# Performance work log

Hardware: AMD Instinct MI355X
Metric: run time of the kernel (lower is better)

Reference implementation:

```python
import jax, jax.numpy as jnp
import numpy as np

TAU = 10.0 / 7.0
V_TH = 1.0
ALPHA = 10.0  # sigmoid surrogate slope

@jax.custom_vjp
def spike_fn(v):
    # Heaviside(v - v_th) forward, sigmoid surrogate backward
    return (v >= V_TH).astype(v.dtype)

def _spike_fwd(v):
    return spike_fn(v), v

def _spike_bwd(v, g):
    s = jax.nn.sigmoid(ALPHA * (v - V_TH))
    return (g * ALPHA * s * (1.0 - s),)

spike_fn.defvjp(_spike_fwd, _spike_bwd)

def lif_multistep(x_bctm):
    # x: [B, C, T, M]; LIF recurrence over T axis, v_reset=0 hard reset,
    # decay_input=True: v = v + (x - v)/tau
    x_t = jnp.moveaxis(x_bctm, 2, 0)  # [T, B, C, M]
    def step(v, x):
        v = v + (x - v) / TAU
        s = spike_fn(v)
        v = v * (1.0 - s)  # hard reset to 0 (not detached)
        return v, s
    v0 = jnp.zeros_like(x_t[0])
    _, s_t = jax.lax.scan(step, v0, x_t)
    return jnp.moveaxis(s_t, 0, 2)  # [B, C, T, M]

def conv2d(x, w, pad, dil):
    return jax.lax.conv_general_dilated(
        x, w, window_strides=(1, 1),
        padding=[(pad[0], pad[0]), (pad[1], pad[1])],
        rhs_dilation=dil,
        dimension_numbers=('NCHW', 'OIHW', 'NCHW'))

def setup_inputs() -> dict:
    key = jax.random.key(0)
    k0, k1, k2, k3, k4 = jax.random.split(key, 5)
    B, T, M = 32, 128, 40
    x = jax.random.normal(k0, (B, 1, T, M), dtype=jnp.float32)
    # kaiming-ish init: std = 1/sqrt(fan_in)
    w1 = jax.random.normal(k1, (64, 1, 4, 3), dtype=jnp.float32) / np.sqrt(1 * 4 * 3)
    w2 = jax.random.normal(k2, (64, 64, 4, 3), dtype=jnp.float32) / np.sqrt(64 * 4 * 3)
    w3 = jax.random.normal(k3, (64, 64, 4, 3), dtype=jnp.float32) / np.sqrt(64 * 4 * 3)
    kw, kb = jax.random.split(k4)
    wf = jax.random.normal(kw, (12, 64 * 40), dtype=jnp.float32) / np.sqrt(64 * 40)
    bf = jnp.zeros((12,), dtype=jnp.float32)
    return {"x": x, "w1": w1, "w2": w2, "w3": w3, "wf": wf, "bf": bf}

def reference(x, w1, w2, w3, wf, bf):
    h = conv2d(x, w1, (2, 1), (1, 1))     # [B,64,T+1,40]
    h = lif_multistep(h)
    h = conv2d(h, w2, (6, 3), (4, 3))     # shape preserved
    h = lif_multistep(h)
    h = conv2d(h, w3, (24, 9), (16, 9))   # shape preserved
    h = lif_multistep(h)
    B, C, T, M = h.shape
    h = jnp.transpose(h, (0, 2, 1, 3)).reshape(B, T, C * M)  # flatten=True path
    y = h @ wf.T + bf                     # [B, T, 12]
    return y.mean(axis=1)                 # [B, 12]
```

## Files before the change

kernel.cpp:

```cpp
#include <hip/hip_runtime.h>


typedef __attribute__((ext_vector_type(8))) _Float16 v8h;
typedef __attribute__((ext_vector_type(16))) float v16f;
typedef _Float16 half_t;

#define NB 32
#define NC 64
#define NT 129
#define TIN 128
#define NM 40
#define MS8 72
#define ROWB8 2952
#define SROWB8 2560

__global__ void prep_wfrag(const float* __restrict__ w, uint4* __restrict__ wf) {
    int tid = blockIdx.x * 256 + threadIdx.x;
    if (tid >= 12288) return;
    int lane = tid & 63;
    int rest = tid >> 6;
    int hl = rest & 1;
    int ct = (rest >> 1) & 1;
    int cq = (rest >> 2) & 3;
    int tap = rest >> 4;
    int kh = tap / 3, kw = tap % 3;
    int co = ct * 32 + (lane & 31);
    unsigned short o[8];
#pragma unroll
    for (int jj = 0; jj < 8; jj++) {
        int ci = cq * 16 + (lane >> 5) * 8 + jj;
        float wv = w[((co * 64 + ci) * 4 + kh) * 3 + kw];
        _Float16 hi = (_Float16)wv;
        _Float16 val = hl ? (_Float16)((wv - (float)hi) * 2048.0f) : hi;
        unsigned short us;
        __builtin_memcpy(&us, &val, 2);
        o[jj] = us;
    }
    uint4 r;
    __builtin_memcpy(&r, o, 16);
    wf[tid] = r;
}

__global__ void conv1_lif1(const float* __restrict__ x, const float* __restrict__ w1,
                           unsigned char* __restrict__ s1) {
    const int mg = blockIdx.x;
    const int b = blockIdx.y;
    const int c = threadIdx.x & 63;
    const int ml = threadIdx.x >> 6;
    const int m = mg * 4 + ml;
    float w[4][3];
#pragma unroll
    for (int kh = 0; kh < 4; kh++)
#pragma unroll
        for (int kw = 0; kw < 3; kw++) w[kh][kw] = w1[(c * 4 + kh) * 3 + kw];
    const float* xb = x + (size_t)b * TIN * NM;

    float xw[12][3];
#pragma unroll
    for (int rr = 0; rr < 12; rr++)
#pragma unroll
        for (int kw = 0; kw < 3; kw++) xw[rr][kw] = 0.f;
#pragma unroll
    for (int rr = 2; rr < 4; rr++)
#pragma unroll
        for (int kw = 0; kw < 3; kw++) {
            int mc = m - 1 + kw;
            xw[rr][kw] = ((unsigned)mc < (unsigned)NM) ? xb[(rr - 2) * NM + mc] : 0.f;
        }

    unsigned char* orow = s1 + ((size_t)b * NT * NM + m) * 64 + c;
    float v = 0.f;
    const float TAUc = 10.0f / 7.0f;

    for (int tb = 0; tb < NT; tb += 8) {
#pragma unroll
        for (int q = 0; q < 8; q++) {
            int row = tb + 2 + q;
#pragma unroll
            for (int kw = 0; kw < 3; kw++) {
                int mc = m - 1 + kw;
                xw[4 + q][kw] = (row < TIN && (unsigned)mc < (unsigned)NM)
                                    ? xb[row * NM + mc] : 0.f;
            }
        }
        int kmax = (NT - tb) < 8 ? (NT - tb) : 8;
#pragma unroll
        for (int k = 0; k < 8; k++) {
            if (k < kmax) {
                float uacc = 0.f;
#pragma unroll
                for (int kh = 0; kh < 4; kh++)
#pragma unroll
                    for (int kw = 0; kw < 3; kw++) uacc += xw[k + kh][kw] * w[kh][kw];
                v = v + (uacc - v) / TAUc;
                orow[(size_t)(tb + k) * NM * 64] = (v >= 1.0f) ? 1 : 0;
                if (v >= 1.0f) v = 0.0f;
            }
        }
#pragma unroll
        for (int rr = 0; rr < 4; rr++)
#pragma unroll
            for (int kw = 0; kw < 3; kw++) xw[rr][kw] = xw[8 + rr][kw];
    }
}

__device__ inline v8h expand01(uint2 raw) {
    unsigned o0 = __builtin_amdgcn_perm(0u, raw.x, 0x04010400u) * 0x3C00u;
    unsigned o1 = __builtin_amdgcn_perm(0u, raw.x, 0x04030402u) * 0x3C00u;
    unsigned o2 = __builtin_amdgcn_perm(0u, raw.y, 0x04010400u) * 0x3C00u;
    unsigned o3 = __builtin_amdgcn_perm(0u, raw.y, 0x04030402u) * 0x3C00u;
    uint4 o = make_uint4(o0, o1, o2, o3);
    return __builtin_bit_cast(v8h, o);
}

template <int DH, int PH, int DW, int PW, int RMOD>
__global__ __launch_bounds__(256, 2) void convW(const unsigned char* __restrict__ spk,
                                                const uint4* __restrict__ wfrag,
                                                float* __restrict__ u) {
    __shared__ uint2 ldsq[7 * ROWB8 / 8];
    char* lds = (char*)ldsq;
    const int tid = threadIdx.x;
    const int lane = tid & 63;
    const int wv = tid >> 6;
    const int wp = wv >> 1;
    const int hl = wv & 1;
    const int bx = blockIdx.x;
    const int b = blockIdx.y;
    int r, jj0;
    if (bx < 32) { r = bx % RMOD; jj0 = (bx / RMOD) * 4; }
    else         { r = 0;         jj0 = (32 / RMOD) * 4; }

    const char* spb = (const char*)spk + (size_t)b * NT * SROWB8;
#pragma unroll
    for (int k = 0; k < 9; k++) {
        int c = tid + k * 256;
        if (c < 2296) {
            int i = c / 328;
            int rem = c - i * 328;
            int s = rem >> 3;
            int q = rem & 7;
            int tg = r - PH + DH * (jj0 + i);
            uint2 val = make_uint2(0u, 0u);
            if ((unsigned)tg < (unsigned)NT && s < 40)
                val = *(const uint2*)(spb + ((size_t)tg * NM + s) * 64 + q * 8);
            *(uint2*)(lds + i * ROWB8 + s * MS8 + q * 8) = val;
        }
    }
    __syncthreads();

    const int pos = lane & 31;
    const int jl = pos >> 4;
    const int ml = pos & 15;
    const int hseg = lane >> 5;
    const int jj = jj0 + 2 * wp + jl;
    const int ldsrow = 2 * wp + jl;
    const int t = r + DH * jj;
    const int mtb[3] = {0, 16, 24};

    int P[3][3];
#pragma unroll
    for (int mt = 0; mt < 3; mt++)
#pragma unroll
        for (int kw = 0; kw < 3; kw++) {
            int md = mtb[mt] + ml + kw * DW - PW;
            int sel = ((unsigned)md < 40u) ? md : 40;
            P[mt][kw] = ldsrow * ROWB8 + sel * MS8 + hseg * 8;
        }

    v16f acc[3][2];
#pragma unroll
    for (int a = 0; a < 3; a++)
#pragma unroll
        for (int c2 = 0; c2 < 2; c2++) acc[a][c2] = (v16f)(0.0f);

    const int hl64 = hl * 64;
    uint4 cA0[4], cA1[4], nA0[4], nA1[4];
#pragma unroll
    for (int cq = 0; cq < 4; cq++) {
        const uint4* wq = wfrag + cq * 256 + hl64 + lane;
        cA0[cq] = wq[0];
        cA1[cq] = wq[128];
    }

#pragma unroll
    for (int tap = 0; tap < 12; tap++) {
        if (tap < 11) {
#pragma unroll
            for (int cq = 0; cq < 4; cq++) {
                const uint4* wq = wfrag + ((tap + 1) * 4 + cq) * 256 + hl64 + lane;
                nA0[cq] = wq[0];
                nA1[cq] = wq[128];
            }
        }
        const int kh = tap / 3, kw = tap % 3;
#pragma unroll
        for (int cq = 0; cq < 4; cq++) {
            uint2 r0 = *(const uint2*)(lds + P[0][kw] + kh * ROWB8 + cq * 16);
            uint2 r1 = *(const uint2*)(lds + P[1][kw] + kh * ROWB8 + cq * 16);
            uint2 r2 = *(const uint2*)(lds + P[2][kw] + kh * ROWB8 + cq * 16);
            v8h B0 = expand01(r0);
            v8h B1 = expand01(r1);
            v8h B2 = expand01(r2);
            v8h A0 = __builtin_bit_cast(v8h, cA0[cq]);
            v8h A1 = __builtin_bit_cast(v8h, cA1[cq]);
            acc[0][0] = __builtin_amdgcn_mfma_f32_32x32x16_f16(A0, B0, acc[0][0], 0, 0, 0);
            acc[0][1] = __builtin_amdgcn_mfma_f32_32x32x16_f16(A1, B0, acc[0][1], 0, 0, 0);
            acc[1][0] = __builtin_amdgcn_mfma_f32_32x32x16_f16(A0, B1, acc[1][0], 0, 0, 0);
            acc[1][1] = __builtin_amdgcn_mfma_f32_32x32x16_f16(A1, B1, acc[1][1], 0, 0, 0);
            acc[2][0] = __builtin_amdgcn_mfma_f32_32x32x16_f16(A0, B2, acc[2][0], 0, 0, 0);
            acc[2][1] = __builtin_amdgcn_mfma_f32_32x32x16_f16(A1, B2, acc[2][1], 0, 0, 0);
        }
        if (tap < 11) {
#pragma unroll
            for (int cq = 0; cq < 4; cq++) {
                cA0[cq] = nA0[cq];
                cA1[cq] = nA1[cq];
            }
        }
    }

    const float invs = 1.0f / 2048.0f;
    float4* lred = (float4*)lds;
    __syncthreads();
#pragma unroll
    for (int mt = 0; mt < 3; mt++) {
        if (hl) {
#pragma unroll
            for (int ct = 0; ct < 2; ct++)
#pragma unroll
                for (int g = 0; g < 4; g++) {
                    float4 vv;
                    vv.x = acc[mt][ct][4 * g + 0];
                    vv.y = acc[mt][ct][4 * g + 1];
                    vv.z = acc[mt][ct][4 * g + 2];
                    vv.w = acc[mt][ct][4 * g + 3];
                    lred[(wp * 8 + ct * 4 + g) * 64 + lane] = vv;
                }
        }
        __syncthreads();
        if (!hl && t < NT) {
            int m = mtb[mt] + ml;
            float* base = u + ((size_t)(b * NT + t) * NM + m) * 64;
#pragma unroll
            for (int ct = 0; ct < 2; ct++)
#pragma unroll
                for (int g = 0; g < 4; g++) {
                    float4 lo = lred[(wp * 8 + ct * 4 + g) * 64 + lane];
                    int co = ct * 32 + 8 * g + 4 * hseg;
                    float4 val;
                    val.x = acc[mt][ct][4 * g + 0] + lo.x * invs;
                    val.y = acc[mt][ct][4 * g + 1] + lo.y * invs;
                    val.z = acc[mt][ct][4 * g + 2] + lo.z * invs;
                    val.w = acc[mt][ct][4 * g + 3] + lo.w * invs;
                    *(float4*)(base + co) = val;
                }
        }
        __syncthreads();
    }
}

__global__ void lif_spikes(const float* __restrict__ u, unsigned char* __restrict__ s2) {
    int tid = blockIdx.x * 256 + threadIdx.x;
    int b = tid / 2560;
    int cm = tid % 2560;
    const float* up = u + (size_t)b * NT * 2560 + cm;
    unsigned char* sp = s2 + (size_t)b * NT * 2560 + cm;
    float v = 0.f;
    const float TAUc = 10.0f / 7.0f;
    for (int tb = 0; tb < 128; tb += 16) {
        float uu[16];
#pragma unroll
        for (int k = 0; k < 16; k++) uu[k] = up[(size_t)(tb + k) * 2560];
#pragma unroll
        for (int k = 0; k < 16; k++) {
            v = v + (uu[k] - v) / TAUc;
            sp[(size_t)(tb + k) * 2560] = (v >= 1.0f) ? 1 : 0;
            if (v >= 1.0f) v = 0.f;
        }
    }
    float uu = up[(size_t)128 * 2560];
    v = v + (uu - v) / TAUc;
    sp[(size_t)128 * 2560] = (v >= 1.0f) ? 1 : 0;
}

__global__ void lif_sum(const float* __restrict__ u, float* __restrict__ hsum) {
    int tid = blockIdx.x * 256 + threadIdx.x;
    int b = tid / 2560;
    int cm = tid % 2560;
    int m = cm >> 6;
    int co = cm & 63;
    const float* up = u + (size_t)b * NT * 2560 + cm;
    float v = 0.f, cnt = 0.f;
    const float TAUc = 10.0f / 7.0f;
    for (int tb = 0; tb < 128; tb += 16) {
        float uu[16];
#pragma unroll
        for (int k = 0; k < 16; k++) uu[k] = up[(size_t)(tb + k) * 2560];
#pragma unroll
        for (int k = 0; k < 16; k++) {
            v = v + (uu[k] - v) / TAUc;
            if (v >= 1.0f) { cnt += 1.0f; v = 0.f; }
        }
    }
    float uu = up[(size_t)128 * 2560];
    v = v + (uu - v) / TAUc;
    if (v >= 1.0f) cnt += 1.0f;
    hsum[b * 2560 + co * NM + m] = cnt;
}

__global__ void fc_out(const float* __restrict__ hsum, const float* __restrict__ wf,
                       const float* __restrict__ bfv, float* __restrict__ out) {
    int b = blockIdx.x;
    int tid = threadIdx.x;
    float p[12];
#pragma unroll
    for (int k = 0; k < 12; k++) p[k] = 0.0f;
    for (int cm = tid; cm < NC * NM; cm += 256) {
        float h = hsum[b * NC * NM + cm];
#pragma unroll
        for (int k = 0; k < 12; k++) p[k] += h * wf[k * (NC * NM) + cm];
    }
    __shared__ float red[12][4];
    int lane = tid & 63, w = tid >> 6;
#pragma unroll
    for (int k = 0; k < 12; k++) {
        float s = p[k];
#pragma unroll
        for (int off = 32; off > 0; off >>= 1) s += __shfl_down(s, off, 64);
        if (lane == 0) red[k][w] = s;
    }
    __syncthreads();
    if (tid < 12) {
        float s = red[tid][0] + red[tid][1] + red[tid][2] + red[tid][3];
        out[b * 12 + tid] = bfv[tid] + s / 129.0f;
    }
}

extern "C" void kernel_launch(void* const* d_in, const int* in_sizes, int n_in,
                              void* d_out, int out_size, void* d_ws, size_t ws_size,
                              hipStream_t stream) {
    const float* x  = (const float*)d_in[0];
    const float* w1 = (const float*)d_in[1];
    const float* w2 = (const float*)d_in[2];
    const float* w3 = (const float*)d_in[3];
    const float* wf = (const float*)d_in[4];
    const float* bf = (const float*)d_in[5];
    float* out = (float*)d_out;

    char* ws = (char*)d_ws;
    unsigned char* s1 = (unsigned char*)ws;
    unsigned char* s2 = (unsigned char*)(ws + 10567680);
    float*  u   = (float*)(ws + 21135360);
    uint4*  wf2 = (uint4*)(ws + 63406080);
    uint4*  wf3 = (uint4*)(ws + 63602688);
    float* hsum = (float*)(ws + 63799296);

    prep_wfrag<<<48, 256, 0, stream>>>(w2, wf2);
    prep_wfrag<<<48, 256, 0, stream>>>(w3, wf3);

    conv1_lif1<<<dim3(10, 32), 256, 0, stream>>>(x, w1, s1);

    convW<4, 6, 3, 3, 4><<<dim3(33, 32), 256, 0, stream>>>(s1, wf2, u);
    lif_spikes<<<320, 256, 0, stream>>>(u, s2);

    convW<16, 24, 9, 9, 16><<<dim3(33, 32), 256, 0, stream>>>(s2, wf3, u);
    lif_sum<<<320, 256, 0, stream>>>(u, hsum);

    fc_out<<<32, 256, 0, stream>>>(hsum, wf, bf, out);
}
```

Before: 224.3 us.

## Double-buffer weight fragment loads via inline asm and merge prep kernels

Replaces the register-prefetch of weight fragments in the conv MFMA loop with a half-tap double-buffered scheme issued as inline global_load_dwordx4 with explicit vmcnt waits. The first weight loads are issued before the LDS barrier so they overlap the spike-tile staging. It also merges the two weight-prep launches into one grid, cutting one launch. This lowers register pressure from holding two full taps of fragments, but manual waitcnt and sched barriers limit compiler scheduling and risk exposing latency.

```diff
diff --git a/kernel.cpp b/kernel.cpp
--- a/kernel.cpp
+++ b/kernel.cpp
@@ -3,6 +3,7 @@
 
 typedef __attribute__((ext_vector_type(8))) _Float16 v8h;
 typedef __attribute__((ext_vector_type(16))) float v16f;
+typedef __attribute__((ext_vector_type(4))) unsigned int u32x4;
 typedef _Float16 half_t;
 
 #define NB 32
@@ -14,8 +15,12 @@
 #define ROWB8 2952
 #define SROWB8 2560
 
-__global__ void prep_wfrag(const float* __restrict__ w, uint4* __restrict__ wf) {
-    int tid = blockIdx.x * 256 + threadIdx.x;
+__global__ void prep_wfrag(const float* __restrict__ w2s, const float* __restrict__ w3s,
+                           uint4* __restrict__ wf2o, uint4* __restrict__ wf3o) {
+    int g = blockIdx.x;
+    const float* w = (g < 48) ? w2s : w3s;
+    uint4* wf = (g < 48) ? wf2o : wf3o;
+    int tid = (g % 48) * 256 + threadIdx.x;
     if (tid >= 12288) return;
     int lane = tid & 63;
     int rest = tid >> 6;
@@ -146,7 +151,6 @@
             *(uint2*)(lds + i * ROWB8 + s * MS8 + q * 8) = val;
         }
     }
-    __syncthreads();
 
     const int pos = lane & 31;
     const int jl = pos >> 4;
@@ -173,36 +177,49 @@
 #pragma unroll
         for (int c2 = 0; c2 < 2; c2++) acc[a][c2] = (v16f)(0.0f);
 
-    const int hl64 = hl * 64;
-    uint4 cA0[4], cA1[4], nA0[4], nA1[4];
-#pragma unroll
-    for (int cq = 0; cq < 4; cq++) {
-        const uint4* wq = wfrag + cq * 256 + hl64 + lane;
-        cA0[cq] = wq[0];
-        cA1[cq] = wq[128];
-    }
-
-#pragma unroll
-    for (int tap = 0; tap < 12; tap++) {
-        if (tap < 11) {
-#pragma unroll
-            for (int cq = 0; cq < 4; cq++) {
-                const uint4* wq = wfrag + ((tap + 1) * 4 + cq) * 256 + hl64 + lane;
-                nA0[cq] = wq[0];
-                nA1[cq] = wq[128];
-            }
-        }
+    unsigned voff0 = (unsigned)(hl * 1024 + lane * 16);
+    unsigned voff1 = voff0 + 4096u;
+    const char* wbp = (const char*)wfrag;
+    u32x4 Ab[2][4];
+
+#define ISSUE4(PAR)                                                                   \
+    {                                                                                 \
+        asm volatile("global_load_dwordx4 %0, %1, %2"                                 \
+                     : "=v"(Ab[PAR][0]) : "v"(voff0), "s"(wbp));                      \
+        asm volatile("global_load_dwordx4 %0, %1, %2 offset:2048"                     \
+                     : "=v"(Ab[PAR][1]) : "v"(voff0), "s"(wbp));                      \
+        asm volatile("global_load_dwordx4 %0, %1, %2"                                 \
+                     : "=v"(Ab[PAR][2]) : "v"(voff1), "s"(wbp));                      \
+        asm volatile("global_load_dwordx4 %0, %1, %2 offset:2048"                     \
+                     : "=v"(Ab[PAR][3]) : "v"(voff1), "s"(wbp));                      \
+        wbp += 8192;                                                                  \
+    }
+
+    ISSUE4(0);
+    __syncthreads();
+
+#pragma unroll
+    for (int s = 0; s < 24; ++s) {
+        const int tap = s >> 1;
         const int kh = tap / 3, kw = tap % 3;
-#pragma unroll
-        for (int cq = 0; cq < 4; cq++) {
+        if (s < 23) {
+            if ((s & 1) == 0) ISSUE4(1) else ISSUE4(0);
+            asm volatile("s_waitcnt vmcnt(4)");
+        } else {
+            asm volatile("s_waitcnt vmcnt(0)");
+        }
+        __builtin_amdgcn_sched_barrier(0);
+#pragma unroll
+        for (int j = 0; j < 2; ++j) {
+            const int cq = (s & 1) * 2 + j;
             uint2 r0 = *(const uint2*)(lds + P[0][kw] + kh * ROWB8 + cq * 16);
             uint2 r1 = *(const uint2*)(lds + P[1][kw] + kh * ROWB8 + cq * 16);
             uint2 r2 = *(const uint2*)(lds + P[2][kw] + kh * ROWB8 + cq * 16);
             v8h B0 = expand01(r0);
             v8h B1 = expand01(r1);
             v8h B2 = expand01(r2);
-            v8h A0 = __builtin_bit_cast(v8h, cA0[cq]);
-            v8h A1 = __builtin_bit_cast(v8h, cA1[cq]);
+            v8h A0 = __builtin_bit_cast(v8h, Ab[s & 1][j * 2 + 0]);
+            v8h A1 = __builtin_bit_cast(v8h, Ab[s & 1][j * 2 + 1]);
             acc[0][0] = __builtin_amdgcn_mfma_f32_32x32x16_f16(A0, B0, acc[0][0], 0, 0, 0);
             acc[0][1] = __builtin_amdgcn_mfma_f32_32x32x16_f16(A1, B0, acc[0][1], 0, 0, 0);
             acc[1][0] = __builtin_amdgcn_mfma_f32_32x32x16_f16(A0, B1, acc[1][0], 0, 0, 0);
@@ -210,14 +227,8 @@
             acc[2][0] = __builtin_amdgcn_mfma_f32_32x32x16_f16(A0, B2, acc[2][0], 0, 0, 0);
             acc[2][1] = __builtin_amdgcn_mfma_f32_32x32x16_f16(A1, B2, acc[2][1], 0, 0, 0);
         }
-        if (tap < 11) {
-#pragma unroll
-            for (int cq = 0; cq < 4; cq++) {
-                cA0[cq] = nA0[cq];
-                cA1[cq] = nA1[cq];
-            }
-        }
-    }
+    }
+#undef ISSUE4
 
     const float invs = 1.0f / 2048.0f;
     float4* lred = (float4*)lds;
@@ -355,8 +366,7 @@
     uint4*  wf3 = (uint4*)(ws + 63602688);
     float* hsum = (float*)(ws + 63799296);
 
-    prep_wfrag<<<48, 256, 0, stream>>>(w2, wf2);
-    prep_wfrag<<<48, 256, 0, stream>>>(w3, wf3);
+    prep_wfrag<<<96, 256, 0, stream>>>(w2, w3, wf2, wf3);
 
     conv1_lif1<<<dim3(10, 32), 256, 0, stream>>>(x, w1, s1);
 
```

Result: faster. 205.2 us (-8.5%).
